# Kernel tuning notes

Measured on AMD Instinct MI355X. Metric: run time of the kernel, lower is better.

## Reference

```python
import jax, jax.numpy as jnp
import numpy as np

N, E, D, K, NCONV = 50000, 800000, 64, 3, 6


def setup_inputs() -> dict:
    key = jax.random.key(0)
    ks = jax.random.split(key, 6)
    X = jax.random.normal(ks[0], (N, D), jnp.float32)
    edge_index = jax.random.randint(ks[1], (2, E), 0, N, dtype=jnp.int64)
    edge_weight = jax.random.uniform(ks[2], (E,), jnp.float32)
    H = jax.random.normal(ks[3], (N, D), jnp.float32)
    lambda_max = jnp.ones((1,), jnp.float32) * 2.0  # typical sym-normalized Laplacian bound
    conv_w = jax.random.normal(ks[4], (NCONV, K, D, D), jnp.float32) / np.sqrt(D)
    conv_b = jnp.zeros((NCONV, D), jnp.float32)
    return {"X": X, "edge_index": edge_index, "edge_weight": edge_weight,
            "H": H, "lambda_max": lambda_max, "conv_w": conv_w, "conv_b": conv_b}


def reference(X, edge_index, edge_weight, H, lambda_max, conv_w, conv_b):
    src, dst = edge_index[0], edge_index[1]
    # symmetric normalization: norm_e = w_e / sqrt(deg_src * deg_dst)
    deg = jax.ops.segment_sum(edge_weight, src, num_segments=N)
    dinv = jnp.where(deg > 0, deg ** -0.5, 0.0)
    norm = edge_weight * dinv[src] * dinv[dst]  # [E]
    lam = lambda_max.reshape(())
    c = 2.0 / lam

    def a_prop(v):  # A_norm @ v via scatter-add over edges, [N,D]
        return jax.ops.segment_sum(norm[:, None] * v[src], dst, num_segments=N)

    def l_hat(v):  # (2/lam)(I - A_norm) v - v
        return (c - 1.0) * v - c * a_prop(v)

    def cheb(v, w, b):  # ChebConv order K: sum_k T_k(L_hat) v @ W_k + b
        tx0, tx1 = v, l_hat(v)
        out = tx0 @ w[0] + tx1 @ w[1]
        for k in range(2, K):
            tx2 = 2.0 * l_hat(tx1) - tx0
            out = out + tx2 @ w[k]
            tx0, tx1 = tx1, tx2
        return out + b

    Z = jax.nn.sigmoid(cheb(X, conv_w[0], conv_b[0]) + cheb(H, conv_w[1], conv_b[1]))
    R = jax.nn.sigmoid(cheb(X, conv_w[2], conv_b[2]) + cheb(H, conv_w[3], conv_b[3]))
    H_tilde = jnp.tanh(cheb(X, conv_w[4], conv_b[4]) + cheb(H * R, conv_w[5], conv_b[5]))
    return Z * H_tilde + (1.0 - Z) * H
```

## Files before the change

### kernel.cpp

```cpp
#include <hip/hip_runtime.h>
#include <cstdint>
#include <cstddef>

typedef unsigned int u32;
typedef unsigned short u16;
typedef unsigned long long u64;

#define D 64
#define NCH 2048
#define CAP 5120

typedef __attribute__((ext_vector_type(8))) short bf16x8;
typedef __attribute__((ext_vector_type(4))) float f32x4;

static __device__ __forceinline__ float sigmoidf_(float x) {
    return 1.f / (1.f + __expf(-x));
}
static __device__ __forceinline__ u16 f2bf(float x) {
    u32 u = __float_as_uint(x);
    return (u16)((u + 0x7fffu + ((u >> 16) & 1u)) >> 16);
}
static __device__ __forceinline__ u32 packbf2(float a, float b) {
    return (u32)f2bf(a) | ((u32)f2bf(b) << 16);
}
static __device__ __forceinline__ float bflo(u32 u) { return __uint_as_float(u << 16); }
static __device__ __forceinline__ float bfhi(u32 u) { return __uint_as_float(u & 0xffff0000u); }


__global__ void init_kernel(u32* cur_d, float* deg, int N_) {
    int i = blockIdx.x * blockDim.x + threadIdx.x;
    if (i < N_) deg[i] = 0.f;
    if (blockIdx.x == 0) cur_d[threadIdx.x] = (u32)(threadIdx.x * CAP);
}

__global__ __launch_bounds__(256) void coarse_kernel(
    const int* __restrict__ src, const int* __restrict__ dst, const float* __restrict__ w,
    u32* cur_d, float* __restrict__ deg,
    u64* __restrict__ slab_d,
    int E, int CE) {
    __shared__ u32 hd[256], cd[256];
    int t = threadIdx.x, c = blockIdx.x;
    hd[t] = 0;
    __syncthreads();
    int e0 = c * CE, e1 = min(E, e0 + CE);
    for (int e = e0 + t; e < e1; e += 256) {
        atomicAdd(&hd[(u32)dst[e] >> 8], 1u);
    }
    __syncthreads();
    cd[t] = atomicAdd(&cur_d[t], hd[t]);
    __syncthreads();
    for (int e = e0 + t; e < e1; e += 256) {
        int s = src[e], d = dst[e];
        float wf = w[e];
        atomicAdd(&deg[s], wf);
        u32 pd = atomicAdd(&cd[(u32)d >> 8], 1u);
        if (pd < (u32)(((d >> 8) + 1) * CAP))
            slab_d[pd] = (u64)((u32)s | (((u32)d & 255u) << 16)) |
                         ((u64)__float_as_uint(wf) << 32);
    }
}

__global__ void bprefix_kernel(const u32* __restrict__ cur_d, u32* __restrict__ bstart, int NB) {
    __shared__ int sd[256];
    int t = threadIdx.x;
    int v = (t < NB) ? min((int)cur_d[t] - t * CAP, CAP) : 0;
    sd[t] = v;
    __syncthreads();
    for (int o = 1; o < 256; o <<= 1) {
        int a = (t >= o) ? sd[t - o] : 0;
        __syncthreads();
        sd[t] += a;
        __syncthreads();
    }
    bstart[t] = (u32)(sd[t] - v);
}

__global__ void dinv_kernel(const float* __restrict__ deg, float* __restrict__ dinv, int N_) {
    int i = blockIdx.x * blockDim.x + threadIdx.x;
    if (i < N_) {
        float dg = deg[i];
        dinv[i] = (dg > 0.f) ? rsqrtf(dg) : 0.f;
    }
}

__global__ __launch_bounds__(256) void fine_dst_kernel(
    const u64* __restrict__ slab, const u32* __restrict__ cur_d,
    const u32* __restrict__ bstart, const float* __restrict__ dinv,
    u32* __restrict__ edge4,
    int* __restrict__ cnt, int* __restrict__ row_start, int N_) {
    __shared__ int h[256], sd[256], cur[256];
    int b = blockIdx.x, t = threadIdx.x;
    int m = min((int)cur_d[b] - b * CAP, CAP);
    const u64* rp = slab + (size_t)b * CAP;
    h[t] = 0;
    __syncthreads();
    for (int i = t; i < m; i += 256) atomicAdd(&h[(int)((rp[i] >> 16) & 255u)], 1);
    __syncthreads();
    int v = h[t];
    sd[t] = v;
    __syncthreads();
    for (int o = 1; o < 256; o <<= 1) {
        int a = (t >= o) ? sd[t - o] : 0;
        __syncthreads();
        sd[t] += a;
        __syncthreads();
    }
    int excl = sd[t] - v;
    cur[t] = excl;
    int bs = (int)bstart[b];
    int node = (b << 8) + t;
    if (node < N_) { cnt[node] = v; row_start[node] = bs + excl; }
    __syncthreads();
    for (int i = t; i < m; i += 256) {
        u64 r = rp[i];
        int f = (int)((r >> 16) & 255u);
        int p = atomicAdd(&cur[f], 1);
        u32 sidx = (u32)(r & 0xffffu);
        float wf = __uint_as_float((u32)(r >> 32));
        float wn = wf * dinv[sidx];
        edge4[bs + p] = sidx | ((u32)f2bf(wn) << 16);
    }
}


__global__ void xh2_kernel(const float* __restrict__ X, const float* __restrict__ H,
                           u32* __restrict__ XH_t, int total) {
    int i = blockIdx.x * blockDim.x + threadIdx.x;
    if (i >= total) return;
    int nn = i >> 6, l = i & 63;
    const float* sp = (l < 32 ? X : H) + (size_t)nn * 64 + ((2 * l) & 63);
    float2 v = *(const float2*)sp;
    XH_t[i] = packbf2(v.x, v.y);
}

__global__ __launch_bounds__(256) void wt_kernel(const float* __restrict__ w, u32* __restrict__ WT) {
    __shared__ float s[64][68];
    int g = blockIdx.x, t = threadIdx.x;
    const float* wp = w + (size_t)g * 4096;
    for (int i = t; i < 1024; i += 256) {
        int k = i >> 4, c4 = (i & 15) * 4;
        *(float4*)&s[k][c4] = *(const float4*)&wp[k * 64 + c4];
    }
    __syncthreads();
    for (int i = t; i < 2048; i += 256) {
        int uk = i & 31, n = i >> 5;
        WT[(size_t)g * 2048 + n * 32 + uk] = packbf2(s[2 * uk][n], s[2 * uk + 1][n]);
    }
}


__global__ __launch_bounds__(256) void lhat128_kernel(
    const u32* __restrict__ vt, const u32* __restrict__ w0t,
    u32* __restrict__ out_t,
    const int* __restrict__ rs, const int* __restrict__ cnt, const float* __restrict__ dinv,
    const u32* __restrict__ edges, const float* __restrict__ lam_ptr, int n) {
    int node = (blockIdx.x * blockDim.x + threadIdx.x) >> 6;
    if (node >= n) return;
    int l = threadIdx.x & 63;
    int g = l >> 4, f = l & 15;
    int e0 = rs[node], end = e0 + cnt[node];
    float acc[8];
#pragma unroll
    for (int j = 0; j < 8; j++) acc[j] = 0.f;

    int base = e0;
    for (; base + 16 <= end; base += 16) {
        u32 r0 = edges[base + g];
        u32 r1 = edges[base + 4 + g];
        u32 r2 = edges[base + 8 + g];
        u32 r3 = edges[base + 12 + g];
        const uint4 q0 = *(const uint4*)(vt + (size_t)(r0 & 0xffffu) * 64 + 4 * f);
        const uint4 q1 = *(const uint4*)(vt + (size_t)(r1 & 0xffffu) * 64 + 4 * f);
        const uint4 q2 = *(const uint4*)(vt + (size_t)(r2 & 0xffffu) * 64 + 4 * f);
        const uint4 q3 = *(const uint4*)(vt + (size_t)(r3 & 0xffffu) * 64 + 4 * f);
        float n0 = __uint_as_float(r0 & 0xffff0000u);
        float n1 = __uint_as_float(r1 & 0xffff0000u);
        float n2 = __uint_as_float(r2 & 0xffff0000u);
        float n3 = __uint_as_float(r3 & 0xffff0000u);
        acc[0] += n0 * bflo(q0.x); acc[1] += n0 * bfhi(q0.x);
        acc[2] += n0 * bflo(q0.y); acc[3] += n0 * bfhi(q0.y);
        acc[4] += n0 * bflo(q0.z); acc[5] += n0 * bfhi(q0.z);
        acc[6] += n0 * bflo(q0.w); acc[7] += n0 * bfhi(q0.w);
        acc[0] += n1 * bflo(q1.x); acc[1] += n1 * bfhi(q1.x);
        acc[2] += n1 * bflo(q1.y); acc[3] += n1 * bfhi(q1.y);
        acc[4] += n1 * bflo(q1.z); acc[5] += n1 * bfhi(q1.z);
        acc[6] += n1 * bflo(q1.w); acc[7] += n1 * bfhi(q1.w);
        acc[0] += n2 * bflo(q2.x); acc[1] += n2 * bfhi(q2.x);
        acc[2] += n2 * bflo(q2.y); acc[3] += n2 * bfhi(q2.y);
        acc[4] += n2 * bflo(q2.z); acc[5] += n2 * bfhi(q2.z);
        acc[6] += n2 * bflo(q2.w); acc[7] += n2 * bfhi(q2.w);
        acc[0] += n3 * bflo(q3.x); acc[1] += n3 * bfhi(q3.x);
        acc[2] += n3 * bflo(q3.y); acc[3] += n3 * bfhi(q3.y);
        acc[4] += n3 * bflo(q3.z); acc[5] += n3 * bfhi(q3.z);
        acc[6] += n3 * bflo(q3.w); acc[7] += n3 * bfhi(q3.w);
    }
    for (; base < end; base += 4) {
        int ei = base + g;
        u32 r0 = (ei < end) ? edges[ei] : 0u;
        const uint4 q0 = *(const uint4*)(vt + (size_t)(r0 & 0xffffu) * 64 + 4 * f);
        float n0 = __uint_as_float(r0 & 0xffff0000u);
        acc[0] += n0 * bflo(q0.x); acc[1] += n0 * bfhi(q0.x);
        acc[2] += n0 * bflo(q0.y); acc[3] += n0 * bfhi(q0.y);
        acc[4] += n0 * bflo(q0.z); acc[5] += n0 * bfhi(q0.z);
        acc[6] += n0 * bflo(q0.w); acc[7] += n0 * bfhi(q0.w);
    }
#pragma unroll
    for (int m = 16; m <= 32; m <<= 1)
#pragma unroll
        for (int j = 0; j < 8; j++) acc[j] += __shfl_xor(acc[j], m);

    const uint4 sv = *(const uint4*)(vt + (size_t)node * 64 + 4 * f);
    float self[8];
    self[0] = bflo(sv.x); self[1] = bfhi(sv.x);
    self[2] = bflo(sv.y); self[3] = bfhi(sv.y);
    self[4] = bflo(sv.z); self[5] = bfhi(sv.z);
    self[6] = bflo(sv.w); self[7] = bfhi(sv.w);
    float c = 2.f / lam_ptr[0];
    float dv = dinv[node];
    float rx[8];
#pragma unroll
    for (int j = 0; j < 8; j++) rx[j] = (c - 1.f) * self[j] - (c * dv) * acc[j];
    if (w0t) {
        const uint4 wv4 = *(const uint4*)(w0t + (size_t)node * 64 + 4 * f);
        rx[0] = 2.f * rx[0] - bflo(wv4.x); rx[1] = 2.f * rx[1] - bfhi(wv4.x);
        rx[2] = 2.f * rx[2] - bflo(wv4.y); rx[3] = 2.f * rx[3] - bfhi(wv4.y);
        rx[4] = 2.f * rx[4] - bflo(wv4.z); rx[5] = 2.f * rx[5] - bfhi(wv4.z);
        rx[6] = 2.f * rx[6] - bflo(wv4.w); rx[7] = 2.f * rx[7] - bfhi(wv4.w);
    }
    if (l < 16) {
        uint4 o;
        o.x = packbf2(rx[0], rx[1]); o.y = packbf2(rx[2], rx[3]);
        o.z = packbf2(rx[4], rx[5]); o.w = packbf2(rx[6], rx[7]);
        *(uint4*)(out_t + (size_t)node * 64 + 4 * f) = o;
    }
}

__global__ __launch_bounds__(256) void lhat64_kernel(
    const u32* __restrict__ vt, const u32* __restrict__ w0t,
    u32* __restrict__ out_t,
    const int* __restrict__ rs, const int* __restrict__ cnt, const float* __restrict__ dinv,
    const u32* __restrict__ edges, const float* __restrict__ lam_ptr, int n) {
    int node = (blockIdx.x * blockDim.x + threadIdx.x) >> 6;
    if (node >= n) return;
    int l = threadIdx.x & 63;
    int g = l >> 3, f = l & 7;
    int e0 = rs[node], end = e0 + cnt[node];
    float acc[8];
#pragma unroll
    for (int j = 0; j < 8; j++) acc[j] = 0.f;

    int base = e0;
    for (; base + 16 <= end; base += 16) {
        u32 r0 = edges[base + g];
        u32 r1 = edges[base + 8 + g];
        const uint4 q0 = *(const uint4*)(vt + (size_t)(r0 & 0xffffu) * 32 + 4 * f);
        const uint4 q1 = *(const uint4*)(vt + (size_t)(r1 & 0xffffu) * 32 + 4 * f);
        float n0 = __uint_as_float(r0 & 0xffff0000u);
        float n1 = __uint_as_float(r1 & 0xffff0000u);
        acc[0] += n0 * bflo(q0.x); acc[1] += n0 * bfhi(q0.x);
        acc[2] += n0 * bflo(q0.y); acc[3] += n0 * bfhi(q0.y);
        acc[4] += n0 * bflo(q0.z); acc[5] += n0 * bfhi(q0.z);
        acc[6] += n0 * bflo(q0.w); acc[7] += n0 * bfhi(q0.w);
        acc[0] += n1 * bflo(q1.x); acc[1] += n1 * bfhi(q1.x);
        acc[2] += n1 * bflo(q1.y); acc[3] += n1 * bfhi(q1.y);
        acc[4] += n1 * bflo(q1.z); acc[5] += n1 * bfhi(q1.z);
        acc[6] += n1 * bflo(q1.w); acc[7] += n1 * bfhi(q1.w);
    }
    for (; base < end; base += 8) {
        int ei = base + g;
        u32 r0 = (ei < end) ? edges[ei] : 0u;
        const uint4 q0 = *(const uint4*)(vt + (size_t)(r0 & 0xffffu) * 32 + 4 * f);
        float n0 = __uint_as_float(r0 & 0xffff0000u);
        acc[0] += n0 * bflo(q0.x); acc[1] += n0 * bfhi(q0.x);
        acc[2] += n0 * bflo(q0.y); acc[3] += n0 * bfhi(q0.y);
        acc[4] += n0 * bflo(q0.z); acc[5] += n0 * bfhi(q0.z);
        acc[6] += n0 * bflo(q0.w); acc[7] += n0 * bfhi(q0.w);
    }
#pragma unroll
    for (int m = 8; m <= 32; m <<= 1)
#pragma unroll
        for (int j = 0; j < 8; j++) acc[j] += __shfl_xor(acc[j], m);

    const uint4 sv = *(const uint4*)(vt + (size_t)node * 32 + 4 * f);
    float self[8];
    self[0] = bflo(sv.x); self[1] = bfhi(sv.x);
    self[2] = bflo(sv.y); self[3] = bfhi(sv.y);
    self[4] = bflo(sv.z); self[5] = bfhi(sv.z);
    self[6] = bflo(sv.w); self[7] = bfhi(sv.w);
    float c = 2.f / lam_ptr[0];
    float dv = dinv[node];
    float rx[8];
#pragma unroll
    for (int j = 0; j < 8; j++) rx[j] = (c - 1.f) * self[j] - (c * dv) * acc[j];
    if (w0t) {
        const uint4 wv4 = *(const uint4*)(w0t + (size_t)node * 32 + 4 * f);
        rx[0] = 2.f * rx[0] - bflo(wv4.x); rx[1] = 2.f * rx[1] - bfhi(wv4.x);
        rx[2] = 2.f * rx[2] - bflo(wv4.y); rx[3] = 2.f * rx[3] - bfhi(wv4.y);
        rx[4] = 2.f * rx[4] - bflo(wv4.z); rx[5] = 2.f * rx[5] - bfhi(wv4.z);
        rx[6] = 2.f * rx[6] - bflo(wv4.w); rx[7] = 2.f * rx[7] - bfhi(wv4.w);
    }
    if (l < 8) {
        uint4 o;
        o.x = packbf2(rx[0], rx[1]); o.y = packbf2(rx[2], rx[3]);
        o.z = packbf2(rx[4], rx[5]); o.w = packbf2(rx[6], rx[7]);
        *(uint4*)(out_t + (size_t)node * 32 + 4 * f) = o;
    }
}

__global__ __launch_bounds__(256) void gemm_gate_kernel(
    const u32* __restrict__ A0, const u32* __restrict__ A1, const u32* __restrict__ A2,
    const u32* __restrict__ WT, const float* __restrict__ convb,
    const float* __restrict__ Hf,
    float* __restrict__ Zb, float* __restrict__ Sh,
    u16* __restrict__ HR_t, int n) {
    __shared__ u32 Ws[64 * 36];
    int t = threadIdx.x;
    int wv = t >> 6, l = t & 63;
    int q = l >> 4, ml = l & 15;
    int R = blockIdx.x * 64 + wv * 16;
    int ar = R + ml; if (ar >= n) ar = n - 1;

    f32x4 S[3][4];
#pragma unroll
    for (int tg = 0; tg < 3; tg++)
#pragma unroll
        for (int ni = 0; ni < 4; ni++) S[tg][ni] = (f32x4){0.f, 0.f, 0.f, 0.f};

    for (int kt = 0; kt < 3; kt++) {
        const u32* Ap = (kt == 0) ? A0 : ((kt == 1) ? A1 : A2);
        const u32* ap = Ap + (size_t)ar * 64 + q * 4;
        bf16x8 af[2][2];
        af[0][0] = *(const bf16x8*)(ap +  0);
        af[1][0] = *(const bf16x8*)(ap + 16);
        af[0][1] = *(const bf16x8*)(ap + 32);
        af[1][1] = *(const bf16x8*)(ap + 48);
#pragma unroll
        for (int cg = 0; cg < 5; cg++) {
            int hf = cg & 1, tg = cg >> 1;
            const u32* Wp = WT + (size_t)(cg * 3 + kt) * 2048;
            __syncthreads();
            {
                int i0 = t * 4, i1 = i0 + 1024;
                uint4 w0 = *(const uint4*)(Wp + i0);
                uint4 w1 = *(const uint4*)(Wp + i1);
                *(uint4*)&Ws[(i0 >> 5) * 36 + (i0 & 31)] = w0;
                *(uint4*)&Ws[(i1 >> 5) * 36 + (i1 & 31)] = w1;
            }
            __syncthreads();
#pragma unroll
            for (int h = 0; h < 2; h++) {
                bf16x8 bw[4];
#pragma unroll
                for (int ni = 0; ni < 4; ni++)
                    bw[ni] = *(const bf16x8*)&Ws[(ni * 16 + ml) * 36 + q * 4 + h * 16];
#pragma unroll
                for (int ni = 0; ni < 4; ni++)
                    S[tg][ni] = __builtin_amdgcn_mfma_f32_16x16x32_bf16(
                        af[h][hf], bw[ni], S[tg][ni], 0, 0, 0);
            }
        }
    }
#pragma unroll
    for (int ni = 0; ni < 4; ni++) {
        int col = ni * 16 + ml;
        float bz = convb[col] + convb[64 + col];
        float br = convb[128 + col] + convb[192 + col];
#pragma unroll
        for (int reg = 0; reg < 4; reg++) {
            int row = R + q * 4 + reg;
            if (row < n) {
                size_t o = (size_t)row * 64 + col;
                float z = sigmoidf_(S[0][ni][reg] + bz);
                float r = sigmoidf_(S[1][ni][reg] + br);
                float hr = Hf[o] * r;
                Zb[o] = z;
                Sh[o] = S[2][ni][reg];
                HR_t[o] = f2bf(hr);
            }
        }
    }
}

__global__ __launch_bounds__(256) void gemm_final_kernel(
    const u32* __restrict__ A0, const u32* __restrict__ A1, const u32* __restrict__ A2,
    const u32* __restrict__ WT, const float* __restrict__ convb,
    const float* __restrict__ Zb, const float* __restrict__ Sh, const float* __restrict__ Hf,
    float* __restrict__ outp, int n) {
    __shared__ u32 Ws[64 * 36];
    int t = threadIdx.x;
    int wv = t >> 6, l = t & 63;
    int q = l >> 4, ml = l & 15;
    int R = blockIdx.x * 64 + wv * 16;
    int ar = R + ml; if (ar >= n) ar = n - 1;

    f32x4 S[4];
#pragma unroll
    for (int ni = 0; ni < 4; ni++) S[ni] = (f32x4){0.f, 0.f, 0.f, 0.f};

    for (int kt = 0; kt < 3; kt++) {
        const u32* Ap = (kt == 0) ? A0 : ((kt == 1) ? A1 : A2);
        const u32* ap = Ap + (size_t)ar * 32 + q * 4;
        bf16x8 af[2];
        af[0] = *(const bf16x8*)(ap +  0);
        af[1] = *(const bf16x8*)(ap + 16);
        const u32* Wp = WT + (size_t)(15 + kt) * 2048;
        __syncthreads();
        {
            int i0 = t * 4, i1 = i0 + 1024;
            uint4 w0 = *(const uint4*)(Wp + i0);
            uint4 w1 = *(const uint4*)(Wp + i1);
            *(uint4*)&Ws[(i0 >> 5) * 36 + (i0 & 31)] = w0;
            *(uint4*)&Ws[(i1 >> 5) * 36 + (i1 & 31)] = w1;
        }
        __syncthreads();
#pragma unroll
        for (int h = 0; h < 2; h++) {
            bf16x8 bw[4];
#pragma unroll
            for (int ni = 0; ni < 4; ni++)
                bw[ni] = *(const bf16x8*)&Ws[(ni * 16 + ml) * 36 + q * 4 + h * 16];
#pragma unroll
            for (int ni = 0; ni < 4; ni++)
                S[ni] = __builtin_amdgcn_mfma_f32_16x16x32_bf16(af[h], bw[ni], S[ni], 0, 0, 0);
        }
    }
#pragma unroll
    for (int ni = 0; ni < 4; ni++) {
        int col = ni * 16 + ml;
        float bh = convb[256 + col] + convb[320 + col];
#pragma unroll
        for (int reg = 0; reg < 4; reg++) {
            int row = R + q * 4 + reg;
            if (row < n) {
                size_t o = (size_t)row * 64 + col;
                float z = Zb[o];
                float ht = tanhf(S[ni][reg] + Sh[o] + bh);
                outp[o] = z * ht + (1.f - z) * Hf[o];
            }
        }
    }
}


extern "C" void kernel_launch(void* const* d_in, const int* in_sizes, int n_in,
                              void* d_out, int out_size, void* d_ws, size_t ws_size,
                              hipStream_t stream) {
    const float* X     = (const float*)d_in[0];
    const int*   ei    = (const int*)d_in[1];
    const float* ew    = (const float*)d_in[2];
    const float* H     = (const float*)d_in[3];
    const float* lam   = (const float*)d_in[4];
    const float* convw = (const float*)d_in[5];
    const float* convb = (const float*)d_in[6];
    float* out = (float*)d_out;

    const int N = in_sizes[0] / D;
    const int E = in_sizes[2];
    const int* src = ei;
    const int* dst = ei + E;

    const int NB = (N + 255) >> 8;
    const int CE = (E + NCH - 1) / NCH;

    char* p = (char*)d_ws;
    auto alloc = [&](size_t bytes) {
        void* r = (void*)p;
        p += (bytes + 255) & ~(size_t)255;
        return r;
    };
    float* Zb   = (float*)alloc((size_t)N * 64 * 4);
    float* Sh   = (float*)alloc((size_t)N * 64 * 4);
    u32* XH_t = (u32*)alloc((size_t)N * 64 * 4);
    u32* T1_t = (u32*)alloc((size_t)N * 64 * 4);
    u32* T2_t = (u32*)alloc((size_t)N * 64 * 4);
    u16* HR_t = (u16*)alloc((size_t)N * 64 * 2);
    u16* U1_t = (u16*)alloc((size_t)N * 64 * 2);
    u16* U2_t = (u16*)alloc((size_t)N * 64 * 2);
    u32* edge4 = (u32*)alloc((size_t)E * 4);
    u64* slab_d = (u64*)alloc((size_t)NB * CAP * 8);
    u32* cur_d  = (u32*)alloc(256 * 4);
    u32* bstart = (u32*)alloc(256 * 4);
    int* cnt       = (int*)alloc((size_t)N * 4);
    int* row_start = (int*)alloc((size_t)N * 4);
    float* deg     = (float*)alloc((size_t)N * 4);
    float* dinv    = (float*)alloc((size_t)N * 4);
    u32* WT = (u32*)alloc((size_t)18 * 2048 * 4);

    const int BLK = 256;
    const int gND  = (N * D + BLK - 1) / BLK;
    const int gNZ  = (N + BLK - 1) / BLK;
    const int gWav = gND;
    const int gx64 = (N + 63) / 64;

    init_kernel<<<gNZ, BLK, 0, stream>>>(cur_d, deg, N);
    coarse_kernel<<<NCH, BLK, 0, stream>>>(src, dst, ew, cur_d, deg, slab_d, E, CE);
    bprefix_kernel<<<1, 256, 0, stream>>>(cur_d, bstart, NB);
    dinv_kernel<<<gNZ, BLK, 0, stream>>>(deg, dinv, N);
    fine_dst_kernel<<<NB, BLK, 0, stream>>>(slab_d, cur_d, bstart, dinv, edge4, cnt, row_start, N);

    wt_kernel<<<18, BLK, 0, stream>>>(convw, WT);
    xh2_kernel<<<gND, BLK, 0, stream>>>(X, H, XH_t, N * D);

    lhat128_kernel<<<gWav, BLK, 0, stream>>>(XH_t, nullptr, T1_t,
                                             row_start, cnt, dinv, edge4, lam, N);
    lhat128_kernel<<<gWav, BLK, 0, stream>>>(T1_t, XH_t, T2_t,
                                             row_start, cnt, dinv, edge4, lam, N);

    gemm_gate_kernel<<<gx64, BLK, 0, stream>>>(XH_t, T1_t, T2_t, WT, convb, H,
                                               Zb, Sh, HR_t, N);

    lhat64_kernel<<<gWav, BLK, 0, stream>>>((const u32*)HR_t, nullptr, (u32*)U1_t,
                                            row_start, cnt, dinv, edge4, lam, N);
    lhat64_kernel<<<gWav, BLK, 0, stream>>>((const u32*)U1_t, (const u32*)HR_t, (u32*)U2_t,
                                            row_start, cnt, dinv, edge4, lam, N);

    gemm_final_kernel<<<gx64, BLK, 0, stream>>>((const u32*)HR_t, (const u32*)U1_t, (const u32*)U2_t,
                                                WT, convb, Zb, Sh, H, out, N);
}
```

Baseline: 346.9 us.

## Bucket edges by source to compute degree without global atomics, merge small kernels

After: 305.8 us. -11.8%, faster.

```diff
diff --git a/kernel.cpp b/kernel.cpp
--- a/kernel.cpp
+++ b/kernel.cpp
@@ -7,8 +7,9 @@
 typedef unsigned long long u64;
 
 #define D 64
-#define NCH 2048
+#define NCH 512
 #define CAP 5120
+#define CPAD 16
 
 typedef __attribute__((ext_vector_type(8))) short bf16x8;
 typedef __attribute__((ext_vector_type(4))) float f32x4;
@@ -27,60 +28,75 @@
 static __device__ __forceinline__ float bfhi(u32 u) { return __uint_as_float(u & 0xffff0000u); }
 
 
-__global__ void init_kernel(u32* cur_d, float* deg, int N_) {
-    int i = blockIdx.x * blockDim.x + threadIdx.x;
-    if (i < N_) deg[i] = 0.f;
-    if (blockIdx.x == 0) cur_d[threadIdx.x] = (u32)(threadIdx.x * CAP);
+__global__ void init_kernel(u32* cur_d, u32* cur_s) {
+    int t = threadIdx.x;
+    cur_d[t * CPAD] = (u32)(t * CAP);
+    cur_s[t * CPAD] = (u32)(t * CAP);
 }
 
 __global__ __launch_bounds__(256) void coarse_kernel(
     const int* __restrict__ src, const int* __restrict__ dst, const float* __restrict__ w,
-    u32* cur_d, float* __restrict__ deg,
-    u64* __restrict__ slab_d,
+    u32* cur_d, u32* cur_s,
+    u64* __restrict__ slab_d, u32* __restrict__ slab_s,
     int E, int CE) {
-    __shared__ u32 hd[256], cd[256];
+    __shared__ u32 hd[256], hs[256], cd[256], cs[256];
     int t = threadIdx.x, c = blockIdx.x;
-    hd[t] = 0;
+    hd[t] = 0; hs[t] = 0;
     __syncthreads();
     int e0 = c * CE, e1 = min(E, e0 + CE);
     for (int e = e0 + t; e < e1; e += 256) {
         atomicAdd(&hd[(u32)dst[e] >> 8], 1u);
-    }
-    __syncthreads();
-    cd[t] = atomicAdd(&cur_d[t], hd[t]);
+        atomicAdd(&hs[(u32)src[e] >> 8], 1u);
+    }
+    __syncthreads();
+    cd[t] = atomicAdd(&cur_d[t * CPAD], hd[t]);
+    cs[t] = atomicAdd(&cur_s[t * CPAD], hs[t]);
     __syncthreads();
     for (int e = e0 + t; e < e1; e += 256) {
         int s = src[e], d = dst[e];
         float wf = w[e];
-        atomicAdd(&deg[s], wf);
         u32 pd = atomicAdd(&cd[(u32)d >> 8], 1u);
+        u32 ps = atomicAdd(&cs[(u32)s >> 8], 1u);
         if (pd < (u32)(((d >> 8) + 1) * CAP))
             slab_d[pd] = (u64)((u32)s | (((u32)d & 255u) << 16)) |
                          ((u64)__float_as_uint(wf) << 32);
-    }
-}
-
-__global__ void bprefix_kernel(const u32* __restrict__ cur_d, u32* __restrict__ bstart, int NB) {
-    __shared__ int sd[256];
+        if (ps < (u32)(((s >> 8) + 1) * CAP))
+            slab_s[ps] = ((u32)s & 255u) | ((u32)f2bf(wf) << 16);
+    }
+}
+
+__global__ __launch_bounds__(256) void fine_deg_bprefix_kernel(
+    const u32* __restrict__ slab_s, const u32* __restrict__ cur_s,
+    const u32* __restrict__ cur_d, float* __restrict__ dinv,
+    u32* __restrict__ bstart, int NB, int N_) {
     int t = threadIdx.x;
-    int v = (t < NB) ? min((int)cur_d[t] - t * CAP, CAP) : 0;
-    sd[t] = v;
-    __syncthreads();
-    for (int o = 1; o < 256; o <<= 1) {
-        int a = (t >= o) ? sd[t - o] : 0;
+    if ((int)blockIdx.x == NB) {
+        __shared__ int sd[256];
+        int v = (t < NB) ? min((int)cur_d[t * CPAD] - t * CAP, CAP) : 0;
+        sd[t] = v;
         __syncthreads();
-        sd[t] += a;
-        __syncthreads();
-    }
-    bstart[t] = (u32)(sd[t] - v);
-}
-
-__global__ void dinv_kernel(const float* __restrict__ deg, float* __restrict__ dinv, int N_) {
-    int i = blockIdx.x * blockDim.x + threadIdx.x;
-    if (i < N_) {
-        float dg = deg[i];
-        dinv[i] = (dg > 0.f) ? rsqrtf(dg) : 0.f;
-    }
+        for (int o = 1; o < 256; o <<= 1) {
+            int a = (t >= o) ? sd[t - o] : 0;
+            __syncthreads();
+            sd[t] += a;
+            __syncthreads();
+        }
+        bstart[t] = (u32)(sd[t] - v);
+        return;
+    }
+    __shared__ float dg[256];
+    int b = blockIdx.x;
+    int m = min((int)cur_s[b * CPAD] - b * CAP, CAP);
+    const u32* rp = slab_s + (size_t)b * CAP;
+    dg[t] = 0.f;
+    __syncthreads();
+    for (int i = t; i < m; i += 256) {
+        u32 r = rp[i];
+        atomicAdd(&dg[r & 255u], __uint_as_float(r & 0xffff0000u));
+    }
+    __syncthreads();
+    int node = (b << 8) + t;
+    if (node < N_) dinv[node] = (dg[t] > 0.f) ? rsqrtf(dg[t]) : 0.f;
 }
 
 __global__ __launch_bounds__(256) void fine_dst_kernel(
@@ -90,7 +106,7 @@
     int* __restrict__ cnt, int* __restrict__ row_start, int N_) {
     __shared__ int h[256], sd[256], cur[256];
     int b = blockIdx.x, t = threadIdx.x;
-    int m = min((int)cur_d[b] - b * CAP, CAP);
+    int m = min((int)cur_d[b * CPAD] - b * CAP, CAP);
     const u64* rp = slab + (size_t)b * CAP;
     h[t] = 0;
     __syncthreads();
@@ -123,29 +139,32 @@
 }
 
 
-__global__ void xh2_kernel(const float* __restrict__ X, const float* __restrict__ H,
-                           u32* __restrict__ XH_t, int total) {
-    int i = blockIdx.x * blockDim.x + threadIdx.x;
+__global__ __launch_bounds__(256) void prep_kernel(
+    const float* __restrict__ X, const float* __restrict__ H,
+    const float* __restrict__ convw,
+    u32* __restrict__ XH_t, u32* __restrict__ WT, int total) {
+    int t = threadIdx.x;
+    if (blockIdx.x < 18) {
+        __shared__ float s[64][68];
+        int g = blockIdx.x;
+        const float* wp = convw + (size_t)g * 4096;
+        for (int i = t; i < 1024; i += 256) {
+            int k = i >> 4, c4 = (i & 15) * 4;
+            *(float4*)&s[k][c4] = *(const float4*)&wp[k * 64 + c4];
+        }
+        __syncthreads();
+        for (int i = t; i < 2048; i += 256) {
+            int uk = i & 31, n = i >> 5;
+            WT[(size_t)g * 2048 + n * 32 + uk] = packbf2(s[2 * uk][n], s[2 * uk + 1][n]);
+        }
+        return;
+    }
+    int i = (blockIdx.x - 18) * 256 + t;
     if (i >= total) return;
     int nn = i >> 6, l = i & 63;
     const float* sp = (l < 32 ? X : H) + (size_t)nn * 64 + ((2 * l) & 63);
     float2 v = *(const float2*)sp;
     XH_t[i] = packbf2(v.x, v.y);
-}
-
-__global__ __launch_bounds__(256) void wt_kernel(const float* __restrict__ w, u32* __restrict__ WT) {
-    __shared__ float s[64][68];
-    int g = blockIdx.x, t = threadIdx.x;
-    const float* wp = w + (size_t)g * 4096;
-    for (int i = t; i < 1024; i += 256) {
-        int k = i >> 4, c4 = (i & 15) * 4;
-        *(float4*)&s[k][c4] = *(const float4*)&wp[k * 64 + c4];
-    }
-    __syncthreads();
-    for (int i = t; i < 2048; i += 256) {
-        int uk = i & 31, n = i >> 5;
-        WT[(size_t)g * 2048 + n * 32 + uk] = packbf2(s[2 * uk][n], s[2 * uk + 1][n]);
-    }
 }
 
 
@@ -478,28 +497,26 @@
     u16* U2_t = (u16*)alloc((size_t)N * 64 * 2);
     u32* edge4 = (u32*)alloc((size_t)E * 4);
     u64* slab_d = (u64*)alloc((size_t)NB * CAP * 8);
-    u32* cur_d  = (u32*)alloc(256 * 4);
+    u32* slab_s = (u32*)alloc((size_t)NB * CAP * 4);
+    u32* cur_d  = (u32*)alloc(256 * CPAD * 4);
+    u32* cur_s  = (u32*)alloc(256 * CPAD * 4);
     u32* bstart = (u32*)alloc(256 * 4);
     int* cnt       = (int*)alloc((size_t)N * 4);
     int* row_start = (int*)alloc((size_t)N * 4);
-    float* deg     = (float*)alloc((size_t)N * 4);
     float* dinv    = (float*)alloc((size_t)N * 4);
     u32* WT = (u32*)alloc((size_t)18 * 2048 * 4);
 
     const int BLK = 256;
     const int gND  = (N * D + BLK - 1) / BLK;
-    const int gNZ  = (N + BLK - 1) / BLK;
     const int gWav = gND;
     const int gx64 = (N + 63) / 64;
 
-    init_kernel<<<gNZ, BLK, 0, stream>>>(cur_d, deg, N);
-    coarse_kernel<<<NCH, BLK, 0, stream>>>(src, dst, ew, cur_d, deg, slab_d, E, CE);
-    bprefix_kernel<<<1, 256, 0, stream>>>(cur_d, bstart, NB);
-    dinv_kernel<<<gNZ, BLK, 0, stream>>>(deg, dinv, N);
+    init_kernel<<<1, 256, 0, stream>>>(cur_d, cur_s);
+    coarse_kernel<<<NCH, BLK, 0, stream>>>(src, dst, ew, cur_d, cur_s, slab_d, slab_s, E, CE);
+    fine_deg_bprefix_kernel<<<NB + 1, BLK, 0, stream>>>(slab_s, cur_s, cur_d, dinv, bstart, NB, N);
     fine_dst_kernel<<<NB, BLK, 0, stream>>>(slab_d, cur_d, bstart, dinv, edge4, cnt, row_start, N);
 
-    wt_kernel<<<18, BLK, 0, stream>>>(convw, WT);
-    xh2_kernel<<<gND, BLK, 0, stream>>>(X, H, XH_t, N * D);
+    prep_kernel<<<18 + gND, BLK, 0, stream>>>(X, H, convw, XH_t, WT, N * D);
 
     lhat128_kernel<<<gWav, BLK, 0, stream>>>(XH_t, nullptr, T1_t,
                                              row_start, cnt, dinv, edge4, lam, N);
```
